# Performance work log

Measured on AMD Instinct MI355X. Metric: run time of the kernel, lower is better.

The kernel has to match this reference:

```python
import jax, jax.numpy as jnp
import numpy as np

N_HEAD = 16
N_EMBD = 2048
HEAD_DIM = N_EMBD // N_HEAD
ROPE_BASE = 10000.0


def _rope_cos_sin(seq_len, dim, dtype):
    inv_freq = 1.0 / (ROPE_BASE ** (jnp.arange(0, dim, 2, dtype=jnp.float32) / dim))
    pos = jnp.arange(seq_len, dtype=jnp.float32)
    freqs = jnp.outer(pos, inv_freq)                 # [T, dim/2]
    emb = jnp.concatenate([freqs, freqs], axis=-1)   # [T, dim]
    return jnp.cos(emb).astype(dtype), jnp.sin(emb).astype(dtype)


def _rotate_half(x):
    x1, x2 = jnp.split(x, 2, axis=-1)
    return jnp.concatenate([-x2, x1], axis=-1)


def _apply_rotary(x, cos, sin):
    # x: [B, H, T, D]; cos/sin: [T, D] broadcast over B,H
    return x * cos[None, None] + _rotate_half(x) * sin[None, None]


def setup_inputs() -> dict:
    key = jax.random.key(0)
    ks = jax.random.split(key, 5)
    B, T, C = 4, 2048, N_EMBD
    s_in = 1.0 / np.sqrt(C)
    return {
        "x": jax.random.normal(ks[0], (B, T, C), dtype=jnp.float32),
        "W_attn": jax.random.normal(ks[1], (C, 3 * C), dtype=jnp.float32) * s_in,
        "b_attn": jax.random.normal(ks[2], (3 * C,), dtype=jnp.float32) * 0.02,
        "W_proj": jax.random.normal(ks[3], (C, C), dtype=jnp.float32) * s_in,
        "b_proj": jax.random.normal(ks[4], (C,), dtype=jnp.float32) * 0.02,
    }


def reference(x, W_attn, b_attn, W_proj, b_proj):
    B, T, C = x.shape
    H, D = N_HEAD, HEAD_DIM
    qkv = x @ W_attn + b_attn                        # [B, T, 3C]
    q, k, v = jnp.split(qkv, 3, axis=2)
    q = q.reshape(B, T, H, D).transpose(0, 2, 1, 3)  # [B, H, T, D]
    k = k.reshape(B, T, H, D).transpose(0, 2, 1, 3)
    v = v.reshape(B, T, H, D).transpose(0, 2, 1, 3)

    cos, sin = _rope_cos_sin(T, D, x.dtype)
    q = _apply_rotary(q, cos, sin)
    k = _apply_rotary(k, cos, sin)

    scale = 1.0 / jnp.sqrt(jnp.asarray(D, dtype=x.dtype))
    scores = jnp.einsum('bhqd,bhkd->bhqk', q, k) * scale
    causal = jnp.tril(jnp.ones((T, T), dtype=bool))
    scores = jnp.where(causal[None, None], scores, jnp.finfo(x.dtype).min)
    attn = jax.nn.softmax(scores, axis=-1)
    y = jnp.einsum('bhqk,bhkd->bhqd', attn, v)       # [B, H, T, D]
    y = y.transpose(0, 2, 1, 3).reshape(B, T, C)
    out = y @ W_proj + b_proj                        # dropout p=0 (eval)
    return out, k, v
```

## Files before the change

### kernel.cpp

```cpp
#include <hip/hip_runtime.h>


typedef __attribute__((ext_vector_type(4))) float f32x4;
typedef __attribute__((ext_vector_type(8))) __bf16 bf16x8;
typedef __attribute__((ext_vector_type(4))) unsigned short us4;

__device__ __forceinline__ unsigned short f2bf(float f) {
  unsigned u = __float_as_uint(f);
  u += 0x7FFFu + ((u >> 16) & 1u);
  return (unsigned short)(u >> 16);
}

__device__ __forceinline__ void gl_lds16(const void* g, void* l) {
  __builtin_amdgcn_global_load_lds(
      (const __attribute__((address_space(1))) void*)g,
      (__attribute__((address_space(3))) void*)l, 16, 0, 0);
}

__device__ __forceinline__ f32x4 mfma_bf16(bf16x8 a, bf16x8 b, f32x4 c) {
  return __builtin_amdgcn_mfma_f32_16x16x32_bf16(a, b, c, 0, 0, 0);
}


__global__ __launch_bounds__(256) void rope_table_kernel(float* __restrict__ cos_t,
                                                         float* __restrict__ sin_t) {
  int idx = blockIdx.x * 256 + threadIdx.x;
  int t = idx >> 6, i = idx & 63;
  float freq = __expf(-(float)i * 0.14391156831212787f);
  float ang = (float)t * freq;
  float s, c;
  sincosf(ang, &s, &c);
  cos_t[idx] = c;
  sin_t[idx] = s;
}

__global__ __launch_bounds__(256) void conv_bf16_kernel(const float* __restrict__ in,
                                                        unsigned short* __restrict__ out,
                                                        int n4) {
  int idx = blockIdx.x * 256 + threadIdx.x;
  int stride = gridDim.x * 256;
  for (; idx < n4; idx += stride) {
    float4 v = ((const float4*)in)[idx];
    us4 o;
    o[0] = f2bf(v.x); o[1] = f2bf(v.y); o[2] = f2bf(v.z); o[3] = f2bf(v.w);
    ((us4*)out)[idx] = o;
  }
}

__global__ __launch_bounds__(256) void transpose_conv_kernel(const float* __restrict__ in,
                                                             unsigned short* __restrict__ out,
                                                             int R, int C, int permute) {
  __shared__ unsigned short tile[64][68];
  const int t = threadIdx.x;
  const int c0 = blockIdx.x * 64, r0 = blockIdx.y * 64;
  const int cq = t & 15, rr = t >> 4;
#pragma unroll
  for (int i = 0; i < 4; ++i) {
    int r = rr + i * 16;
    float4 v = *(const float4*)&in[(size_t)(r0 + r) * C + c0 + cq * 4];
    tile[r][cq * 4 + 0] = f2bf(v.x);
    tile[r][cq * 4 + 1] = f2bf(v.y);
    tile[r][cq * 4 + 2] = f2bf(v.z);
    tile[r][cq * 4 + 3] = f2bf(v.w);
  }
  __syncthreads();
#pragma unroll
  for (int ii = 0; ii < 4; ++ii) {
    int c = rr + ii * 16;
    int n = c0 + c;
    int np = n;
    if (permute && n < 4096) {
      int d = n & 127, blk = d >> 5;
      int dd = (blk == 1) ? d + 32 : (blk == 2) ? d - 32 : d;
      np = (n & ~127) | dd;
    }
    us4 o;
#pragma unroll
    for (int jj = 0; jj < 4; ++jj) o[jj] = tile[cq * 4 + jj][c];
    *(us4*)&out[(size_t)np * R + r0 + cq * 4] = o;
  }
}


#define BARR __builtin_amdgcn_s_barrier()
#define LGKM                                                                   \
  do {                                                                         \
    asm volatile("s_waitcnt lgkmcnt(0)" ::: "memory");                         \
    __builtin_amdgcn_sched_barrier(0);                                         \
  } while (0)
#define WAITV(N) asm volatile("s_waitcnt vmcnt(" #N ")" ::: "memory")

#define STAGE_A_HALF(BUF, T, H)                                                \
  do {                                                                         \
    const int k0_ = (T) * 64;                                                  \
    _Pragma("unroll") for (int i_ = 0; i_ < 2; ++i_) {                         \
      int c_ = i_ * 512 + tid;                                                 \
      int rp_ = c_ >> 3, s_ = c_ & 7;                                          \
      int row_ = (rp_ & 63) + (H) * 64 + (rp_ >> 6) * 128;                     \
      gl_lds16(Ag + (size_t)row_ * 2048 + k0_ + ((s_ ^ (row_ & 7)) << 3),      \
               &As[BUF][row_ * 64 + s_ * 8]);                                  \
    }                                                                          \
  } while (0)

#define STAGE_B_HALF(BUF, T, H)                                                \
  do {                                                                         \
    const int k0_ = (T) * 64;                                                  \
    _Pragma("unroll") for (int i_ = 0; i_ < 2; ++i_) {                         \
      int c_ = i_ * 512 + tid;                                                 \
      int rp_ = c_ >> 3, s_ = c_ & 7;                                          \
      int row_ = (rp_ & 31) + (H) * 32 + (rp_ >> 5) * 64;                      \
      gl_lds16(Bg + (size_t)row_ * 2048 + k0_ + ((s_ ^ (row_ & 7)) << 3),      \
               &Bs[BUF][row_ * 64 + s_ * 8]);                                  \
    }                                                                          \
  } while (0)

#define LDA(mh)                                                                \
  _Pragma("unroll") for (int m2_ = 0; m2_ < 4; ++m2_)                          \
  _Pragma("unroll") for (int kk_ = 0; kk_ < 2; ++kk_) {                        \
    int R_ = wm * 128 + (mh) * 64 + m2_ * 16 + ln;                             \
    av[m2_][kk_] = *(const bf16x8*)&Ab[R_ * 64 +                               \
        (((kk_ * 64 + g * 16) ^ ((R_ & 7) << 4)) >> 1)];                       \
  }

#define LDB2                                                                   \
  _Pragma("unroll") for (int nh_ = 0; nh_ < 2; ++nh_)                          \
  _Pragma("unroll") for (int n2_ = 0; n2_ < 2; ++n2_)                          \
  _Pragma("unroll") for (int kk_ = 0; kk_ < 2; ++kk_) {                        \
    int R_ = wn * 64 + nh_ * 32 + n2_ * 16 + ln;                               \
    bv[nh_ * 2 + n2_][kk_] = *(const bf16x8*)&Bb[R_ * 64 +                     \
        (((kk_ * 64 + g * 16) ^ ((R_ & 7) << 4)) >> 1)];                       \
  }

#define MF16(mh, nh)                                                           \
  do {                                                                         \
    __builtin_amdgcn_s_setprio(1);                                             \
    _Pragma("unroll") for (int m2_ = 0; m2_ < 4; ++m2_)                        \
    _Pragma("unroll") for (int n2_ = 0; n2_ < 2; ++n2_)                        \
    _Pragma("unroll") for (int kk_ = 0; kk_ < 2; ++kk_)                        \
      acc[(mh) * 4 + m2_][(nh) * 2 + n2_] = mfma_bf16(                         \
          av[m2_][kk_], bv[(nh) * 2 + n2_][kk_],                               \
          acc[(mh) * 4 + m2_][(nh) * 2 + n2_]);                                \
    __builtin_amdgcn_s_setprio(0);                                             \
  } while (0)

#define GEMM_ENGINE_4PH(NT)                                                    \
  STAGE_A_HALF(0, 0, 0); STAGE_B_HALF(0, 0, 0);                                \
  STAGE_B_HALF(0, 0, 1); STAGE_A_HALF(0, 0, 1);                                \
  for (int t = 0; t < (NT); ++t) {                                             \
    const int p_ = t & 1, q_ = p_ ^ 1;                                         \
    const unsigned short* Ab = &As[p_][0];                                     \
    const unsigned short* Bb = &Bs[p_][0];                                     \
    const bool pf_ = (t + 1 < (NT));                                           \
    WAITV(2);                                                                  \
    BARR;                                                                      \
                                \
    LDB2; LDA(0);                                                              \
    if (pf_) STAGE_A_HALF(q_, t + 1, 0);                                       \
    LGKM;                                                                      \
    MF16(0, 0);                                                                \
                                             \
    if (pf_) STAGE_B_HALF(q_, t + 1, 0);                                       \
    MF16(0, 1);                                                                \
    if (pf_) { WAITV(4); } else { WAITV(0); }                                  \
    BARR;                                                                      \
                                        \
    LDA(1);                                                                    \
    if (pf_) STAGE_B_HALF(q_, t + 1, 1);                                       \
    LGKM;                                                                      \
    MF16(1, 0);                                                                \
                                             \
    if (pf_) STAGE_A_HALF(q_, t + 1, 1);                                       \
    MF16(1, 1);                                                                \
  }

__global__ __launch_bounds__(512, 2) void gemm_qkv_kernel(
    const unsigned short* __restrict__ xbf, const unsigned short* __restrict__ wt,
    const float* __restrict__ bias, const float* __restrict__ cost,
    const float* __restrict__ sint, float* __restrict__ out_k,
    float* __restrict__ out_v, unsigned short* __restrict__ qbf,
    unsigned short* __restrict__ kbf, unsigned short* __restrict__ vtb) {
  __shared__ __attribute__((aligned(16))) unsigned short As[2][256 * 64];
  __shared__ __attribute__((aligned(16))) unsigned short Bs[2][256 * 64];
  const int tid = threadIdx.x;
  const int wid = tid >> 6, l = tid & 63, g = l >> 4, ln = l & 15;
  const int wm = wid >> 2, wn = wid & 3;
  const int xcd = blockIdx.x & 7, local = blockIdx.x >> 3;
  const int mtile = xcd * 4 + (local & 3);
  const int ntile = local >> 2;
  const unsigned short* Ag = xbf + (size_t)(mtile * 256) * 2048;
  const unsigned short* Bg = wt + (size_t)(ntile * 256) * 2048;

  f32x4 acc[8][4];
#pragma unroll
  for (int i = 0; i < 8; ++i)
#pragma unroll
    for (int j = 0; j < 4; ++j) acc[i][j] = (f32x4){0.f, 0.f, 0.f, 0.f};
  bf16x8 av[4][2], bv[4][2];

  GEMM_ENGINE_4PH(32);

  const int colb = ntile * 256 + wn * 64;
  const int p = colb >> 11;
  const int h = (colb >> 7) & 15;
  const int Mb = mtile * 256 + wm * 128;

  if (p == 2) {
    float bvv[4];
#pragma unroll
    for (int nf = 0; nf < 4; ++nf) bvv[nf] = bias[colb + nf * 16 + ln];
    const int dbase = (wn & 1) * 64;
#pragma unroll
    for (int mf = 0; mf < 8; ++mf) {
      int t0 = Mb + mf * 16 + g * 4;
      int b = t0 >> 11, t = t0 & 2047;
      const int z = b * 16 + h;
      size_t base = ((size_t)z * 2048 + t) * 128;
      size_t vtz = (size_t)z * (128 * 2048);
#pragma unroll
      for (int nf = 0; nf < 4; ++nf) {
        int d = dbase + nf * 16 + ln;
        us4 pack;
#pragma unroll
        for (int r = 0; r < 4; ++r) {
          float val = acc[mf][nf][r] + bvv[nf];
          out_v[base + (size_t)r * 128 + d] = val;
          pack[r] = f2bf(val);
        }
        *(us4*)&vtb[vtz + (size_t)d * 2048 + t] = pack;
      }
    }
  } else {
    const float sc2 = 0.12751743681128098f;
    const int half32 = (wn & 1) * 32;
    float blo[2], bhi[2];
#pragma unroll
    for (int nf = 0; nf < 2; ++nf) {
      int d_lo = half32 + nf * 16 + ln;
      blo[nf] = bias[p * 2048 + h * 128 + d_lo];
      bhi[nf] = bias[p * 2048 + h * 128 + d_lo + 64];
    }
#pragma unroll
    for (int mf = 0; mf < 8; ++mf)
#pragma unroll
      for (int r = 0; r < 4; ++r) {
        int m = Mb + mf * 16 + g * 4 + r;
        int b = m >> 11, t = m & 2047;
        size_t base = ((size_t)(b * 16 + h) * 2048 + t) * 128;
#pragma unroll
        for (int nf = 0; nf < 2; ++nf) {
          int d_lo = half32 + nf * 16 + ln;
          float cv = cost[t * 64 + d_lo], sv = sint[t * 64 + d_lo];
          float a = acc[mf][nf][r] + blo[nf];
          float bq = acc[mf][nf + 2][r] + bhi[nf];
          float lo = a * cv - bq * sv;
          float hi = bq * cv + a * sv;
          if (p == 0) {
            qbf[base + d_lo] = f2bf(lo * sc2);
            qbf[base + d_lo + 64] = f2bf(hi * sc2);
          } else {
            out_k[base + d_lo] = lo;
            out_k[base + d_lo + 64] = hi;
            kbf[base + d_lo] = f2bf(lo);
            kbf[base + d_lo + 64] = f2bf(hi);
          }
        }
      }
  }
}

__global__ __launch_bounds__(512, 2) void gemm_proj_kernel(
    const unsigned short* __restrict__ ybf, const unsigned short* __restrict__ wpt,
    const float* __restrict__ bias, float* __restrict__ out) {
  __shared__ __attribute__((aligned(16))) unsigned short As[2][256 * 64];
  __shared__ __attribute__((aligned(16))) unsigned short Bs[2][256 * 64];
  const int tid = threadIdx.x;
  const int wid = tid >> 6, l = tid & 63, g = l >> 4, ln = l & 15;
  const int wm = wid >> 2, wn = wid & 3;
  const int xcd = blockIdx.x & 7, local = blockIdx.x >> 3;
  const int mtile = xcd * 4 + (local & 3);
  const int ntile = local >> 2;
  const unsigned short* Ag = ybf + (size_t)(mtile * 256) * 2048;
  const unsigned short* Bg = wpt + (size_t)(ntile * 256) * 2048;

  f32x4 acc[8][4];
#pragma unroll
  for (int i = 0; i < 8; ++i)
#pragma unroll
    for (int j = 0; j < 4; ++j) acc[i][j] = (f32x4){0.f, 0.f, 0.f, 0.f};
  bf16x8 av[4][2], bv[4][2];

  GEMM_ENGINE_4PH(32);

  const int n0 = ntile * 256 + wn * 64;
  const int Mb = mtile * 256 + wm * 128;
  float bvv[4];
#pragma unroll
  for (int nf = 0; nf < 4; ++nf) bvv[nf] = bias[n0 + nf * 16 + ln];
#pragma unroll
  for (int mf = 0; mf < 8; ++mf)
#pragma unroll
    for (int r = 0; r < 4; ++r) {
      int m = Mb + mf * 16 + g * 4 + r;
      size_t rb = (size_t)m * 2048 + n0;
#pragma unroll
      for (int nf = 0; nf < 4; ++nf)
        out[rb + nf * 16 + ln] = acc[mf][nf][r] + bvv[nf];
    }
}

__global__ __launch_bounds__(256, 2) void attn_kernel(
    const unsigned short* __restrict__ qbf, const unsigned short* __restrict__ kbf,
    const unsigned short* __restrict__ vtbf, unsigned short* __restrict__ ybf) {
  __shared__ __attribute__((aligned(16))) unsigned short Ks[2][64 * 128];
  __shared__ __attribute__((aligned(16))) unsigned short Vs[2][128 * 64];
  __shared__ __attribute__((aligned(16))) __bf16 Ps[4][32 * 64];
  const int tid = threadIdx.x;
  const int w = tid >> 6, l = tid & 63, g = l >> 4, ln = l & 15;
  const int bid = blockIdx.x;
  const int z = (bid & 7) * 8 + ((bid >> 3) & 7);
  const int qp = 15 - (bid >> 6);
  const size_t zo = (size_t)z * (2048 * 128);
  const size_t zv = (size_t)z * (128 * 2048);
  const int Q0w = qp * 128 + w * 32;
  const int jn = 2 * qp + 2;
  const int jlw = 2 * qp + (w >> 1);
  __bf16* Pw = Ps[w];

  bf16x8 qv[2][4];
#pragma unroll
  for (int mf = 0; mf < 2; ++mf)
#pragma unroll
    for (int kk = 0; kk < 4; ++kk)
      qv[mf][kk] = *(const bf16x8*)
          &qbf[zo + (size_t)(Q0w + mf * 16 + ln) * 128 + kk * 32 + g * 8];

  f32x4 o[2][8];
#pragma unroll
  for (int mf = 0; mf < 2; ++mf)
#pragma unroll
    for (int nf = 0; nf < 8; ++nf) o[mf][nf] = (f32x4){0.f, 0.f, 0.f, 0.f};
  float mrun[2][4], lrun[2][4];
#pragma unroll
  for (int mf = 0; mf < 2; ++mf)
#pragma unroll
    for (int r = 0; r < 4; ++r) { mrun[mf][r] = -3e38f; lrun[mf][r] = 0.f; }

#define STAGE_KV(J, B)                                                         \
  do {                                                                         \
    const int kv0_ = (J) << 6;                                                 \
    _Pragma("unroll") for (int i_ = 0; i_ < 4; ++i_) {                         \
      int c_ = i_ * 256 + tid;                                                 \
      int r_ = c_ >> 4, s_ = c_ & 15;                                          \
      gl_lds16(kbf + zo + (size_t)(kv0_ + r_) * 128 +                          \
                   (((s_ * 16) ^ ((r_ & 7) << 4)) >> 1),                       \
               &Ks[B][c_ * 8]);                                                \
    }                                                                          \
    _Pragma("unroll") for (int i_ = 0; i_ < 4; ++i_) {                         \
      int c_ = i_ * 256 + tid;                                                 \
      int d_ = c_ >> 3, s_ = c_ & 7;                                           \
      gl_lds16(vtbf + zv + (size_t)d_ * 2048 + kv0_ +                          \
                   (((s_ * 16) ^ ((d_ & 7) << 4)) >> 1),                       \
               &Vs[B][c_ * 8]);                                                \
    }                                                                          \
  } while (0)

  STAGE_KV(0, 0);
  STAGE_KV(1, 1);

  for (int j = 0; j < jn; ++j) {
    if (j + 1 < jn)
      asm volatile("s_waitcnt vmcnt(8)" ::: "memory");
    else
      asm volatile("s_waitcnt vmcnt(0)" ::: "memory");
    __builtin_amdgcn_s_barrier();
    const int bfr = j & 1;
    const unsigned short* Kb = Ks[bfr];
    const unsigned short* Vb = Vs[bfr];

    if (j <= jlw) {
      const int kv0 = j << 6;
      f32x4 s[2][4];
#pragma unroll
      for (int mf = 0; mf < 2; ++mf)
#pragma unroll
        for (int nf = 0; nf < 4; ++nf) s[mf][nf] = (f32x4){0.f, 0.f, 0.f, 0.f};
#pragma unroll
      for (int kk = 0; kk < 4; ++kk) {
        bf16x8 kf[4];
#pragma unroll
        for (int nf = 0; nf < 4; ++nf) {
          int rr = nf * 16 + ln;
          kf[nf] = *(const bf16x8*)
              &Kb[rr * 128 + (((kk * 64 + g * 16) ^ ((rr & 7) << 4)) >> 1)];
        }
#pragma unroll
        for (int mf = 0; mf < 2; ++mf)
#pragma unroll
          for (int nf = 0; nf < 4; ++nf)
            s[mf][nf] = mfma_bf16(qv[mf][kk], kf[nf], s[mf][nf]);
      }

      if (j == jlw) {
#pragma unroll
        for (int mf = 0; mf < 2; ++mf)
#pragma unroll
          for (int nf = 0; nf < 4; ++nf)
#pragma unroll
            for (int r = 0; r < 4; ++r)
              if (kv0 + nf * 16 + ln > Q0w + mf * 16 + g * 4 + r)
                s[mf][nf][r] = -3e38f;
      }

      float mx[2][4];
#pragma unroll
      for (int mf = 0; mf < 2; ++mf)
#pragma unroll
        for (int r = 0; r < 4; ++r) {
          float m0 = fmaxf(fmaxf(s[mf][0][r], s[mf][1][r]),
                           fmaxf(s[mf][2][r], s[mf][3][r]));
          m0 = fmaxf(m0, __shfl_xor(m0, 1));
          m0 = fmaxf(m0, __shfl_xor(m0, 2));
          m0 = fmaxf(m0, __shfl_xor(m0, 4));
          m0 = fmaxf(m0, __shfl_xor(m0, 8));
          mx[mf][r] = m0;
        }

      float dm = 0.f;
#pragma unroll
      for (int mf = 0; mf < 2; ++mf)
#pragma unroll
        for (int r = 0; r < 4; ++r) dm = fmaxf(dm, mx[mf][r] - mrun[mf][r]);
      if (__any(dm > 11.5416f)) {
#pragma unroll
        for (int mf = 0; mf < 2; ++mf)
#pragma unroll
          for (int r = 0; r < 4; ++r) {
            float mn = fmaxf(mrun[mf][r], mx[mf][r]);
            float al = exp2f(mrun[mf][r] - mn);
            mrun[mf][r] = mn;
            lrun[mf][r] *= al;
#pragma unroll
            for (int nf = 0; nf < 8; ++nf) o[mf][nf][r] *= al;
          }
      }

#pragma unroll
      for (int mf = 0; mf < 2; ++mf)
#pragma unroll
        for (int r = 0; r < 4; ++r) {
          const float m0 = mrun[mf][r];
          const int row_l = mf * 16 + g * 4 + r;
          float rs = 0.f;
#pragma unroll
          for (int nf = 0; nf < 4; ++nf) {
            float pv = exp2f(s[mf][nf][r] - m0);
            rs += pv;
            int byte = ((nf * 16 + ln) << 1) ^ ((row_l & 7) << 4);
            Pw[row_l * 64 + (byte >> 1)] = (__bf16)pv;
          }
          rs += __shfl_xor(rs, 1);
          rs += __shfl_xor(rs, 2);
          rs += __shfl_xor(rs, 4);
          rs += __shfl_xor(rs, 8);
          lrun[mf][r] += rs;
        }

      asm volatile("s_waitcnt lgkmcnt(0)" ::: "memory");
      __builtin_amdgcn_sched_barrier(0);

#pragma unroll
      for (int kk2 = 0; kk2 < 2; ++kk2) {
        bf16x8 pa[2];
#pragma unroll
        for (int mf = 0; mf < 2; ++mf) {
          int pr = mf * 16 + ln;
          int byte = (kk2 * 64 + g * 16) ^ ((pr & 7) << 4);
          pa[mf] = *(const bf16x8*)&Pw[pr * 64 + (byte >> 1)];
        }
#pragma unroll
        for (int nf2 = 0; nf2 < 8; ++nf2) {
          int dr = nf2 * 16 + ln;
          bf16x8 vf = *(const bf16x8*)
              &Vb[dr * 64 + (((kk2 * 64 + g * 16) ^ ((dr & 7) << 4)) >> 1)];
#pragma unroll
          for (int mf = 0; mf < 2; ++mf)
            o[mf][nf2] = mfma_bf16(pa[mf], vf, o[mf][nf2]);
        }
      }
    }

    __builtin_amdgcn_s_barrier();
    __builtin_amdgcn_sched_barrier(0);
    if (j + 2 < jn) STAGE_KV(j + 2, bfr);
  }
#undef STAGE_KV

  const int b = z >> 4, h = z & 15;
#pragma unroll
  for (int mf = 0; mf < 2; ++mf)
#pragma unroll
    for (int r = 0; r < 4; ++r) {
      float inv = 1.f / lrun[mf][r];
      int t = Q0w + mf * 16 + g * 4 + r;
      size_t rb = ((size_t)b * 2048 + t) * 2048 + h * 128;
#pragma unroll
      for (int nf2 = 0; nf2 < 8; ++nf2)
        ybf[rb + nf2 * 16 + ln] = f2bf(o[mf][nf2][r] * inv);
    }
}

extern "C" void kernel_launch(void* const* d_in, const int* in_sizes, int n_in,
                              void* d_out, int out_size, void* d_ws, size_t ws_size,
                              hipStream_t stream) {
  (void)in_sizes; (void)n_in; (void)out_size; (void)ws_size;
  const float* x      = (const float*)d_in[0];
  const float* W_attn = (const float*)d_in[1];
  const float* b_attn = (const float*)d_in[2];
  const float* W_proj = (const float*)d_in[3];
  const float* b_proj = (const float*)d_in[4];

  float* out   = (float*)d_out;
  float* out_k = out + 16777216;
  float* out_v = out + 33554432;

  char* ws = (char*)d_ws;
  unsigned short* q_bf  = (unsigned short*)(ws + 0);
  unsigned short* k_bf  = (unsigned short*)(ws + 33554432);
  unsigned short* vt_bf = (unsigned short*)(ws + 67108864);
  unsigned short* x_bf  = (unsigned short*)(ws + 100663296);
  unsigned short* y2d   = x_bf;
  unsigned short* wt    = (unsigned short*)(ws + 134217728);
  unsigned short* wpt   = (unsigned short*)(ws + 159383552);
  float* cos_t = (float*)(ws + 167772160);
  float* sin_t = (float*)(ws + 168296448);

  rope_table_kernel<<<512, 256, 0, stream>>>(cos_t, sin_t);
  conv_bf16_kernel<<<2048, 256, 0, stream>>>(x, x_bf, 16777216 / 4);
  transpose_conv_kernel<<<dim3(6144 / 64, 2048 / 64), 256, 0, stream>>>(W_attn, wt, 2048, 6144, 1);
  transpose_conv_kernel<<<dim3(2048 / 64, 2048 / 64), 256, 0, stream>>>(W_proj, wpt, 2048, 2048, 0);
  gemm_qkv_kernel<<<768, 512, 0, stream>>>(x_bf, wt, b_attn, cos_t, sin_t,
                                           out_k, out_v, q_bf, k_bf, vt_bf);
  attn_kernel<<<1024, 256, 0, stream>>>(q_bf, k_bf, vt_bf, y2d);
  gemm_proj_kernel<<<256, 512, 0, stream>>>(y2d, wpt, b_proj, out);
}
```

Before: 469.1 us.

## Stage V transpose through LDS for coalesced stores; raise priority around MFMA

In the QKV GEMM epilogue for the V part, each warp now writes its bf16-packed tile into a swizzled region of the reused A/B shared buffers, then reads it back row-wise. This lets the transposed V^T output be written to global memory as contiguous 16-byte vectors instead of scattered 8-byte stores with a 2048-element stride. Separately, the attention kernel wraps its QK and PV MFMA blocks in s_setprio(1)/s_setprio(0) so that waves issuing matrix math get scheduling priority. The cost is an extra __syncthreads plus an LDS round trip in the epilogue, and the priority hint could delay other waves' memory or softmax work.

```diff
diff --git a/kernel.cpp b/kernel.cpp
--- a/kernel.cpp
+++ b/kernel.cpp
@@ -4,6 +4,7 @@
 typedef __attribute__((ext_vector_type(4))) float f32x4;
 typedef __attribute__((ext_vector_type(8))) __bf16 bf16x8;
 typedef __attribute__((ext_vector_type(4))) unsigned short us4;
+typedef __attribute__((ext_vector_type(8))) unsigned short us8;
 
 __device__ __forceinline__ unsigned short f2bf(float f) {
   unsigned u = __float_as_uint(f);
@@ -205,6 +206,9 @@
   const int Mb = mtile * 256 + wm * 128;
 
   if (p == 2) {
+    __syncthreads();
+    unsigned short* reg = (wid < 4) ? &As[0][0] + wid * 8192
+                                    : &Bs[0][0] + (wid - 4) * 8192;
     float bvv[4];
 #pragma unroll
     for (int nf = 0; nf < 4; ++nf) bvv[nf] = bias[colb + nf * 16 + ln];
@@ -212,22 +216,32 @@
 #pragma unroll
     for (int mf = 0; mf < 8; ++mf) {
       int t0 = Mb + mf * 16 + g * 4;
-      int b = t0 >> 11, t = t0 & 2047;
-      const int z = b * 16 + h;
-      size_t base = ((size_t)z * 2048 + t) * 128;
-      size_t vtz = (size_t)z * (128 * 2048);
+      int bb = t0 >> 11, tt = t0 & 2047;
+      size_t base = ((size_t)(bb * 16 + h) * 2048 + tt) * 128;
 #pragma unroll
       for (int nf = 0; nf < 4; ++nf) {
-        int d = dbase + nf * 16 + ln;
+        int dl = nf * 16 + ln;
         us4 pack;
 #pragma unroll
         for (int r = 0; r < 4; ++r) {
           float val = acc[mf][nf][r] + bvv[nf];
-          out_v[base + (size_t)r * 128 + d] = val;
+          out_v[base + (size_t)r * 128 + dbase + dl] = val;
           pack[r] = f2bf(val);
         }
-        *(us4*)&vtb[vtz + (size_t)d * 2048 + t] = pack;
+        int byt = (mf * 32 + g * 8) ^ ((dl & 7) << 4);
+        *(us4*)&reg[dl * 128 + (byt >> 1)] = pack;
       }
+    }
+    asm volatile("s_waitcnt lgkmcnt(0)" ::: "memory");
+    __builtin_amdgcn_sched_barrier(0);
+    const size_t vtz = (size_t)((Mb >> 11) * 16 + h) * (128 * 2048);
+    const int tbase = (Mb & 2047);
+#pragma unroll
+    for (int it = 0; it < 16; ++it) {
+      int dl = it * 4 + (l >> 4);
+      int byt = ((l & 15) * 16) ^ ((dl & 7) << 4);
+      us8 v8 = *(const us8*)&reg[dl * 128 + (byt >> 1)];
+      *(us8*)&vtb[vtz + (size_t)(dbase + dl) * 2048 + tbase + (l & 15) * 8] = v8;
     }
   } else {
     const float sc2 = 0.12751743681128098f;
@@ -393,11 +407,13 @@
           kf[nf] = *(const bf16x8*)
               &Kb[rr * 128 + (((kk * 64 + g * 16) ^ ((rr & 7) << 4)) >> 1)];
         }
+        __builtin_amdgcn_s_setprio(1);
 #pragma unroll
         for (int mf = 0; mf < 2; ++mf)
 #pragma unroll
           for (int nf = 0; nf < 4; ++nf)
             s[mf][nf] = mfma_bf16(qv[mf][kk], kf[nf], s[mf][nf]);
+        __builtin_amdgcn_s_setprio(0);
       }
 
       if (j == jlw) {
@@ -477,6 +493,7 @@
           int byte = (kk2 * 64 + g * 16) ^ ((pr & 7) << 4);
           pa[mf] = *(const bf16x8*)&Pw[pr * 64 + (byte >> 1)];
         }
+        __builtin_amdgcn_s_setprio(1);
 #pragma unroll
         for (int nf2 = 0; nf2 < 8; ++nf2) {
           int dr = nf2 * 16 + ln;
@@ -486,6 +503,7 @@
           for (int mf = 0; mf < 2; ++mf)
             o[mf][nf2] = mfma_bf16(pa[mf], vf, o[mf][nf2]);
         }
+        __builtin_amdgcn_s_setprio(0);
       }
     }
 
```

Result: faster. 458.8 us (-2.2%).
